# Kernel optimization log

Measured on AMD Instinct MI355X. Metric: run time of the kernel, lower is better.

The kernel has to match this reference:

```python
import jax, jax.numpy as jnp
import numpy as np

B_, C_, H_, W_ = 16, 128, 64, 64
D_MODEL = C_ // 4          # 32
D_STATE = 16
D_CONV = 4
EXPAND = 2
D_INNER = EXPAND * D_MODEL # 64
DT_RANK = (D_MODEL + 15) // 16  # 2
EPS = 1e-5


def setup_inputs() -> dict:
    key = jax.random.key(0)
    ks = jax.random.split(key, 8)
    def n(k, shape, scale=0.02):
        return jax.random.normal(k, shape, dtype=jnp.float32) * scale
    A = jnp.broadcast_to(jnp.arange(1, D_STATE + 1, dtype=jnp.float32), (D_INNER, D_STATE))
    return {
        "input":     jax.random.normal(ks[0], (B_, C_, H_, W_), dtype=jnp.float32),
        "ln_g":      jnp.ones((C_,), jnp.float32),
        "ln_b":      jnp.zeros((C_,), jnp.float32),
        "in_proj_w": n(ks[1], (2 * D_INNER, D_MODEL)),
        "conv_w":    n(ks[2], (D_INNER, D_CONV), 0.1),
        "conv_b":    jnp.zeros((D_INNER,), jnp.float32),
        "x_proj_w":  n(ks[3], (DT_RANK + 2 * D_STATE, D_INNER)),
        "dt_proj_w": n(ks[4], (D_INNER, DT_RANK), 0.5),
        "dt_proj_b": jnp.full((D_INNER,), -4.6, jnp.float32),  # softplus^-1(~0.01)
        "A_log":     jnp.log(A),
        "D":         jnp.ones((D_INNER,), jnp.float32),
        "out_proj_w": n(ks[5], (D_MODEL, D_INNER)),
    }


def _mamba(x, in_proj_w, conv_w, conv_b, x_proj_w, dt_proj_w, dt_proj_b, A_log, D, out_proj_w):
    # x: (G, L, d_model); G = 4 chunks * batch, shared weights -> one big batched call
    G, L, _ = x.shape
    xz = jnp.einsum('gld,ed->gle', x, in_proj_w)          # (G, L, 2*d_inner)
    xi, z = jnp.split(xz, 2, axis=-1)
    # causal depthwise conv1d along L
    xc = jax.lax.conv_general_dilated(
        xi.transpose(0, 2, 1),                            # (G, d_inner, L)
        conv_w[:, None, :],                               # (d_inner, 1, k)
        window_strides=(1,), padding=[(D_CONV - 1, 0)],
        feature_group_count=D_INNER)
    u = jax.nn.silu(xc.transpose(0, 2, 1) + conv_b)       # (G, L, d_inner)
    x_dbl = jnp.einsum('gld,ed->gle', u, x_proj_w)        # (G, L, dt_rank + 2*d_state)
    dt, Bm, Cm = jnp.split(x_dbl, [DT_RANK, DT_RANK + D_STATE], axis=-1)
    delta = jax.nn.softplus(jnp.einsum('glr,dr->gld', dt, dt_proj_w) + dt_proj_b)
    A = -jnp.exp(A_log)                                   # (d_inner, d_state)

    def step(h, inputs):
        d_t, u_t, B_t, C_t = inputs                       # (G,d) (G,d) (G,n) (G,n)
        dA = jnp.exp(d_t[..., None] * A)                  # (G, d, n)
        h = h * dA + (d_t * u_t)[..., None] * B_t[:, None, :]
        y = jnp.einsum('gdn,gn->gd', h, C_t)
        return h, y

    h0 = jnp.zeros((G, D_INNER, D_STATE), x.dtype)
    xs = (delta.transpose(1, 0, 2), u.transpose(1, 0, 2),
          Bm.transpose(1, 0, 2), Cm.transpose(1, 0, 2))
    _, ys = jax.lax.scan(step, h0, xs)                    # ys: (L, G, d_inner)
    y = ys.transpose(1, 0, 2) + u * D
    y = y * jax.nn.silu(z)
    return jnp.einsum('gld,ed->gle', y, out_proj_w)       # (G, L, d_model)


def reference(input, ln_g, ln_b, in_proj_w, conv_w, conv_b, x_proj_w,
              dt_proj_w, dt_proj_b, A_log, D, out_proj_w):
    B, C, H, W = input.shape
    L = H * W
    xf = input.reshape(B, C, L).transpose(0, 2, 1)        # (B, L, C)
    mu = xf.mean(-1, keepdims=True)
    var = ((xf - mu) ** 2).mean(-1, keepdims=True)
    xn = (xf - mu) / jnp.sqrt(var + EPS) * ln_g + ln_b
    # chunk channels into 4 groups (torch.chunk dim=2) and batch them for one mamba call
    chunks = xn.reshape(B, L, 4, C // 4).transpose(2, 0, 1, 3).reshape(4 * B, L, C // 4)
    y = chunks + _mamba(chunks, in_proj_w, conv_w, conv_b, x_proj_w,
                        dt_proj_w, dt_proj_b, A_log, D, out_proj_w)
    out = y.reshape(4, B, L, C // 4).transpose(1, 2, 0, 3).reshape(B, L, C)
    return out.transpose(0, 2, 1).reshape(B, C, H, W)
```

## Files before the change

kernel.cpp:

```cpp
#include <hip/hip_runtime.h>
#include <hip/hip_bf16.h>
#include <hip/hip_fp16.h>
#include <math.h>

typedef __hip_bfloat16 bf;
typedef float f2 __attribute__((ext_vector_type(2)));
typedef _Float16 hf2 __attribute__((ext_vector_type(2)));

#define BB   16
#define CC   128
#define LL   4096
#define DM   32
#define DI   64
#define DSN  16
#define GG   64
#define NC   128
#define CL   32
#define TLV  61
#define NT   68
#define XS   133
#define YS   35
#define XROW 20

__device__ __forceinline__ float bf2f(bf x) { return __bfloat162float(x); }
__device__ __forceinline__ bf f2bf(float x) { return __float2bfloat16(x); }
__device__ __forceinline__ float blo(unsigned v) { return __uint_as_float(v << 16); }
__device__ __forceinline__ float bhi(unsigned v) { return __uint_as_float(v & 0xffff0000u); }
__device__ __forceinline__ float us2f(unsigned short v) { return __uint_as_float((unsigned)v << 16); }
__device__ __forceinline__ unsigned pack2(float a, float b) {
  bf ba = f2bf(a), bb = f2bf(b);
  unsigned short ua = *(unsigned short*)&ba, ub = *(unsigned short*)&bb;
  return (unsigned)ua | ((unsigned)ub << 16);
}
__device__ __forceinline__ unsigned pack2h(float a, float b) {
  _Float16 ha = (_Float16)a, hb = (_Float16)b;
  unsigned short ua = *(unsigned short*)&ha, ub = *(unsigned short*)&hb;
  return (unsigned)ua | ((unsigned)ub << 16);
}
__device__ __forceinline__ hf2 u2h2(unsigned v) {
  union { unsigned u; hf2 h; } c; c.u = v; return c.h;
}

#if __has_builtin(__builtin_amdgcn_exp2f)
#define EXP2F(x) __builtin_amdgcn_exp2f(x)
#else
#define EXP2F(x) exp2f(x)
#endif

#if __has_builtin(__builtin_amdgcn_fdot2)
#define FDOT2(a, b, c) __builtin_amdgcn_fdot2((a), (b), (c), false)
#else
#define FDOT2(a, b, c) ((c) + (float)(a).x * (float)(b).x + (float)(a).y * (float)(b).y)
#endif

__device__ __forceinline__ float sigmoidf_(float x) { return 1.0f / (1.0f + __expf(-x)); }
__device__ __forceinline__ float softplus_fast(float x) {
  float t = EXP2F(-fabsf(x) * 1.44269504088896f);
  return fmaxf(x, 0.0f) + 0.69314718056f * __log2f(1.0f + t);
}

__global__ __launch_bounds__(256, 4) void k1_ln_conv(
    const float* __restrict__ input, const float* __restrict__ ln_g, const float* __restrict__ ln_b,
    const float* __restrict__ in_proj_w, const float* __restrict__ conv_w, const float* __restrict__ conv_b,
    bf* __restrict__ u_ws, bf* __restrict__ xn_ws) {
  __shared__ unsigned ldsbuf[8960];
  __shared__ float mu_s[64], rs_s[64];
  float* xnT = (float*)ldsbuf;
  unsigned short* xiS = (unsigned short*)ldsbuf;
  int b = blockIdx.x / NT;
  int tile = blockIdx.x - b * NT;
  int l0 = tile * TLV;
  int tid = threadIdx.x;
  const float* inb = input + (size_t)b * CC * LL;
#pragma unroll
  for (int k = 0; k < 32; k++) {
    int i = tid + k * 256;
    int j = i & 63, c = i >> 6;
    int l = l0 - 3 + j;
    xnT[j * XS + c] = (l >= 0 && l < LL) ? inb[c * LL + l] : 0.0f;
  }
  __syncthreads();
  if (tid < 64) {
    float s = 0.f, s2 = 0.f;
    for (int c = 0; c < CC; c++) { float v = xnT[tid * XS + c]; s += v; s2 = fmaf(v, v, s2); }
    float mu = s * (1.0f / CC);
    float var = s2 * (1.0f / CC) - mu * mu;
    mu_s[tid] = mu;
    rs_s[tid] = rsqrtf(var + 1e-5f);
  }
  __syncthreads();
#pragma unroll
  for (int k = 0; k < 32; k++) {
    int i = tid + k * 256;
    int j = i & 63, c = i >> 6;
    xnT[j * XS + c] = (xnT[j * XS + c] - mu_s[j]) * rs_s[j] * ln_g[c] + ln_b[c];
  }
  __syncthreads();
  for (int i = tid; i < CC * TLV; i += 256) {
    int c = i / TLV, j2 = i - c * TLV;
    int l = l0 + j2;
    if (l < LL) xn_ws[((size_t)(b * CC + c)) * LL + l] = f2bf(xnT[(j2 + 3) * XS + c]);
  }
  int g = tid >> 6, j = tid & 63;
  float xr[32];
#pragma unroll
  for (int r = 0; r < 32; r++) xr[r] = xnT[j * XS + g * DM + r];
  bool zero_col = (l0 - 3 + j < 0);
  __syncthreads();
#pragma unroll
  for (int c2 = 0; c2 < 4; c2++) {
    float acc[16];
#pragma unroll
    for (int dd = 0; dd < 16; dd++) {
      const float* w = in_proj_w + (c2 * 16 + dd) * DM;
      float a = 0.f;
#pragma unroll
      for (int r = 0; r < 32; r++) a = fmaf(xr[r], w[r], a);
      acc[dd] = zero_col ? 0.f : a;
    }
    unsigned* xo = (unsigned*)&ldsbuf[(g * 64 + j) * YS + c2 * 8];
#pragma unroll
    for (int k = 0; k < 8; k++)
      xo[k] = pack2(acc[2 * k], acc[2 * k + 1]);
  }
  __syncthreads();
  int d = j;
  float cw0 = conv_w[d * 4 + 0], cw1 = conv_w[d * 4 + 1];
  float cw2 = conv_w[d * 4 + 2], cw3 = conv_w[d * 4 + 3];
  float cb = conv_b[d];
  bf* uo = u_ws + (size_t)(g * BB + b) * LL * DI + d;
  float x3 = 0.f, x2 = 0.f, x1 = 0.f, x0 = 0.f;
  for (int jj = 0; jj < 64; jj++) {
    float xi = us2f(xiS[(g * 64 + jj) * (2 * YS) + d]);
    x3 = x2; x2 = x1; x1 = x0; x0 = xi;
    int l = l0 + jj - 3;
    if (jj >= 3 && l < LL) {
      float pre = x3 * cw0 + x2 * cw1 + x1 * cw2 + x0 * cw3 + cb;
      float uu = pre * sigmoidf_(pre);
      uo[(size_t)l * DI] = f2bf(uu);
    }
  }
}

__global__ __launch_bounds__(256) void k2_xproj(
    const bf* __restrict__ u_ws, const float* __restrict__ x_proj_w,
    unsigned* __restrict__ xdbl) {
  __shared__ unsigned uS[256 * 33];
  int tid = threadIdx.x;
  size_t pos0 = (size_t)blockIdx.x * 256;
  const unsigned* src = (const unsigned*)u_ws + pos0 * 32;
#pragma unroll
  for (int k = 0; k < 32; k++) {
    int idx = tid + k * 256;
    uS[(idx >> 5) * 33 + (idx & 31)] = src[idx];
  }
  __syncthreads();
  float xdb[34];
#pragma unroll
  for (int e = 0; e < 34; e++) xdb[e] = 0.f;
#pragma unroll
  for (int c2 = 0; c2 < 4; c2++) {
    float f[16];
#pragma unroll
    for (int k = 0; k < 8; k++) {
      unsigned v = uS[tid * 33 + c2 * 8 + k];
      f[2 * k] = blo(v); f[2 * k + 1] = bhi(v);
    }
#pragma unroll
    for (int e = 0; e < 34; e++) {
      const float* w = x_proj_w + e * DI + c2 * 16;
      float a = xdb[e];
#pragma unroll
      for (int i = 0; i < 16; i++) a = fmaf(f[i], w[i], a);
      xdb[e] = a;
    }
  }
  unsigned* row = &uS[tid * 33];
  row[0] = pack2(xdb[0], xdb[1]);
#pragma unroll
  for (int n = 0; n < 8; n++) row[4 + n]  = pack2h(xdb[2 + 2 * n], xdb[3 + 2 * n]);
#pragma unroll
  for (int n = 0; n < 8; n++) row[12 + n] = pack2h(xdb[18 + 2 * n], xdb[19 + 2 * n]);
  __syncthreads();
  unsigned* dst = xdbl + pos0 * XROW;
#pragma unroll
  for (int k = 0; k < XROW; k++) {
    int idx = tid + k * 256;
    int r = idx / XROW, c = idx - r * XROW;
    dst[idx] = uS[r * 33 + c];
  }
}

__device__ __forceinline__ bool ladder_check(const float* A_log, int d, float a0) {
  bool ok = true;
#pragma unroll
  for (int n = 1; n < DSN; n++) {
    float an = -__expf(A_log[d * DSN + n]) * 1.44269504088896f;
    ok = ok && (fabsf(an / a0 - (float)(n + 1)) < 1e-3f);
  }
  return ok;
}

__global__ __launch_bounds__(256, 8) void k3_scanA(
    const unsigned* __restrict__ xdbl, const bf* __restrict__ u_ws,
    const float* __restrict__ A_log, const float* __restrict__ dt_proj_w,
    const float* __restrict__ dt_proj_b,
    __half* __restrict__ hloc, __half* __restrict__ ssum_ws) {
  __shared__ __align__(16) unsigned bS3[4 * 256];
  __shared__ unsigned dtS3[4 * 32];
  int tid = threadIdx.x;
  int wv = __builtin_amdgcn_readfirstlane(tid >> 6);
  int wid = __builtin_amdgcn_readfirstlane(blockIdx.x * 4 + wv);
  int s = wid >> 7, chunk = wid & (NC - 1);
  int d = tid & 63;
  float a0 = -__expf(A_log[d * DSN]) * 1.44269504088896f;
  bool ok = ladder_check(A_log, d, a0);
  float w0 = dt_proj_w[2 * d], w1 = dt_proj_w[2 * d + 1], bd = dt_proj_b[d];
  hf2 h2[8];
#pragma unroll
  for (int p2 = 0; p2 < 8; p2++) h2[p2] = u2h2(0u);
  float ss = 0.f;
  size_t base = (size_t)s * LL + (size_t)chunk * CL;
  const unsigned short* up = (const unsigned short*)u_ws + base * DI + d;
  const unsigned* xrow = xdbl + base * XROW;
  int wb = wv * 256, wd3 = wv * 32;
#pragma unroll
  for (int k = 0; k < 4; k++) {
    int jj2 = k * 64 + d;
    bS3[wb + jj2] = xrow[(jj2 >> 3) * XROW + 4 + (jj2 & 7)];
  }
  if (d < 32) dtS3[wd3 + d] = xrow[d * XROW];
  if (ok) {
    for (int t = 0; t < CL; t++) {
      unsigned dtp = dtS3[wd3 + t];
      uint4 bA = *(const uint4*)&bS3[wb + t * 8];
      uint4 bB = *(const uint4*)&bS3[wb + t * 8 + 4];
      float x = fmaf(bhi(dtp), w1, fmaf(blo(dtp), w0, bd));
      float delta = softplus_fast(x);
      float uu = us2f(up[(size_t)t * DI]);
      float du = delta * uu;
      ss += delta;
      float E = EXP2F(delta * a0);
      float E2 = E * E;
      hf2 e2; e2.x = (_Float16)E; e2.y = (_Float16)E2;
      hf2 E22; E22.x = (_Float16)E2; E22.y = (_Float16)E2;
      _Float16 duh = (_Float16)du;
      hf2 du2; du2.x = duh; du2.y = duh;
      unsigned bw[8] = {bA.x, bA.y, bA.z, bA.w, bB.x, bB.y, bB.z, bB.w};
#pragma unroll
      for (int p2 = 0; p2 < 8; p2++) {
        hf2 Bp = u2h2(bw[p2]);
        h2[p2] = h2[p2] * e2 + Bp * du2;
        e2 = e2 * E22;
      }
    }
  } else {
    f2 A2p[8];
#pragma unroll
    for (int p2 = 0; p2 < 8; p2++) {
      A2p[p2].x = -__expf(A_log[d * DSN + 2 * p2]) * 1.44269504088896f;
      A2p[p2].y = -__expf(A_log[d * DSN + 2 * p2 + 1]) * 1.44269504088896f;
    }
    for (int t = 0; t < CL; t++) {
      unsigned dtp = dtS3[wd3 + t];
      uint4 bA = *(const uint4*)&bS3[wb + t * 8];
      uint4 bB = *(const uint4*)&bS3[wb + t * 8 + 4];
      float x = fmaf(bhi(dtp), w1, fmaf(blo(dtp), w0, bd));
      float delta = softplus_fast(x);
      float uu = us2f(up[(size_t)t * DI]);
      float du = delta * uu;
      ss += delta;
      _Float16 duh = (_Float16)du;
      hf2 du2; du2.x = duh; du2.y = duh;
      unsigned bw[8] = {bA.x, bA.y, bA.z, bA.w, bB.x, bB.y, bB.z, bB.w};
#pragma unroll
      for (int p2 = 0; p2 < 8; p2++) {
        hf2 ee; ee.x = (_Float16)EXP2F(delta * A2p[p2].x); ee.y = (_Float16)EXP2F(delta * A2p[p2].y);
        hf2 Bp = u2h2(bw[p2]);
        h2[p2] = h2[p2] * ee + Bp * du2;
      }
    }
  }
  size_t ob = (size_t)wid * (DSN * DI) + d;
  unsigned short* hl = (unsigned short*)hloc;
#pragma unroll
  for (int n = 0; n < DSN; n++) {
    _Float16 v = (n & 1) ? h2[n >> 1].y : h2[n >> 1].x;
    hl[ob + n * DI] = *(unsigned short*)&v;
  }
  ssum_ws[wid * DI + d] = __float2half(ss);
}

__global__ __launch_bounds__(256) void k4_combine(
    const __half* __restrict__ ssum_ws, const float* __restrict__ A_log, __half* hloc_hin) {
  int s = blockIdx.x >> 2;
  int q = blockIdx.x & 3;
  int tid = threadIdx.x;
  int n = q * 4 + (tid >> 6);
  int d = tid & 63;
  float A2 = -__expf(A_log[d * DSN + n]) * 1.44269504088896f;
  float h = 0.f;
  const __half* sp = ssum_ws + (size_t)s * NC * DI + d;
  __half* hp = hloc_hin + (size_t)s * NC * (DSN * DI) + n * DI + d;
  float hl[4], ssv[4], hln[4], ssn[4];
#pragma unroll
  for (int j = 0; j < 4; j++) {
    hln[j] = __half2float(hp[(size_t)j * (DSN * DI)]);
    ssn[j] = __half2float(sp[j * DI]);
  }
  for (int kb = 0; kb < NC / 4; kb++) {
#pragma unroll
    for (int j = 0; j < 4; j++) { hl[j] = hln[j]; ssv[j] = ssn[j]; }
    if (kb + 1 < NC / 4) {
#pragma unroll
      for (int j = 0; j < 4; j++) {
        int k = (kb + 1) * 4 + j;
        hln[j] = __half2float(hp[(size_t)k * (DSN * DI)]);
        ssn[j] = __half2float(sp[k * DI]);
      }
    }
#pragma unroll
    for (int j = 0; j < 4; j++) {
      int k = kb * 4 + j;
      float ap = EXP2F(A2 * ssv[j]);
      hp[(size_t)k * (DSN * DI)] = __float2half(h);
      h = fmaf(h, ap, hl[j]);
    }
  }
}

__global__ __launch_bounds__(512, 4) void k56_scan_final(
    const unsigned* __restrict__ xdbl, const bf* __restrict__ u_ws,
    const float* __restrict__ A_log, const float* __restrict__ dt_proj_w,
    const float* __restrict__ dt_proj_b, const float* __restrict__ Dw,
    const __half* __restrict__ hin, const bf* __restrict__ xn_ws,
    const float* __restrict__ in_proj_w, const float* __restrict__ out_proj_w,
    float* __restrict__ out) {
  __shared__ unsigned y2S[4 * 64 * 33];
  __shared__ __align__(16) unsigned bcS[8 * 512];
  __shared__ unsigned dtS[8 * 32];
  int b = blockIdx.x >> 6;
  int cpair = blockIdx.x & 63;
  int l0b = cpair * 64;
  int tid = threadIdx.x;
  int w = __builtin_amdgcn_readfirstlane(tid >> 6);
  int g = w >> 1, half = w & 1;
  int d = tid & 63;
  int chunk = cpair * 2 + half;
  int s_u = __builtin_amdgcn_readfirstlane(g * BB + b);
  float a0 = -__expf(A_log[d * DSN]) * 1.44269504088896f;
  bool ok = ladder_check(A_log, d, a0);
  float w0 = dt_proj_w[2 * d], w1 = dt_proj_w[2 * d + 1], bd = dt_proj_b[d];
  float Dd = Dw[d];
  size_t hb = (size_t)(s_u * NC + chunk) * (DSN * DI) + d;
  const unsigned short* hinus = (const unsigned short*)hin;
  hf2 h2[8];
#pragma unroll
  for (int p2 = 0; p2 < 8; p2++) {
    unsigned lo = hinus[hb + (size_t)(2 * p2) * DI];
    unsigned hi = hinus[hb + (size_t)(2 * p2 + 1) * DI];
    h2[p2] = u2h2(lo | (hi << 16));
  }
  size_t base = (size_t)s_u * LL + (size_t)chunk * CL;
  const unsigned short* up = (const unsigned short*)u_ws + base * DI + d;
  const unsigned* xrow = xdbl + base * XROW;
  int wbc = w * 512, wdt = w * 32;
#pragma unroll
  for (int k = 0; k < 8; k++) {
    int jj2 = k * 64 + d;
    bcS[wbc + jj2] = xrow[(jj2 >> 4) * XROW + 4 + (jj2 & 15)];
  }
  if (d < 32) dtS[wdt + d] = xrow[d * XROW];
  unsigned short* yout = (unsigned short*)y2S + g * 4224 + (half * CL) * 66 + d;
  if (ok) {
    for (int t = 0; t < CL; t++) {
      unsigned dtp = dtS[wdt + t];
      uint4 bA = *(const uint4*)&bcS[wbc + t * 16];
      uint4 bB = *(const uint4*)&bcS[wbc + t * 16 + 4];
      uint4 cA = *(const uint4*)&bcS[wbc + t * 16 + 8];
      uint4 cB = *(const uint4*)&bcS[wbc + t * 16 + 12];
      float x = fmaf(bhi(dtp), w1, fmaf(blo(dtp), w0, bd));
      float delta = softplus_fast(x);
      float uu = us2f(up[(size_t)t * DI]);
      float du = delta * uu;
      float E = EXP2F(delta * a0);
      float E2 = E * E;
      hf2 e2; e2.x = (_Float16)E; e2.y = (_Float16)E2;
      hf2 E22; E22.x = (_Float16)E2; E22.y = (_Float16)E2;
      _Float16 duh = (_Float16)du;
      hf2 du2; du2.x = duh; du2.y = duh;
      float yacc = 0.f;
      unsigned bw[8] = {bA.x, bA.y, bA.z, bA.w, bB.x, bB.y, bB.z, bB.w};
      unsigned cw[8] = {cA.x, cA.y, cA.z, cA.w, cB.x, cB.y, cB.z, cB.w};
#pragma unroll
      for (int p2 = 0; p2 < 8; p2++) {
        hf2 Bp = u2h2(bw[p2]);
        hf2 Cp = u2h2(cw[p2]);
        h2[p2] = h2[p2] * e2 + Bp * du2;
        yacc = FDOT2(h2[p2], Cp, yacc);
        e2 = e2 * E22;
      }
      bf rv = f2bf(yacc + uu * Dd);
      yout[t * 66] = *(unsigned short*)&rv;
    }
  } else {
    f2 A2p[8];
#pragma unroll
    for (int p2 = 0; p2 < 8; p2++) {
      A2p[p2].x = -__expf(A_log[d * DSN + 2 * p2]) * 1.44269504088896f;
      A2p[p2].y = -__expf(A_log[d * DSN + 2 * p2 + 1]) * 1.44269504088896f;
    }
    for (int t = 0; t < CL; t++) {
      unsigned dtp = dtS[wdt + t];
      uint4 bA = *(const uint4*)&bcS[wbc + t * 16];
      uint4 bB = *(const uint4*)&bcS[wbc + t * 16 + 4];
      uint4 cA = *(const uint4*)&bcS[wbc + t * 16 + 8];
      uint4 cB = *(const uint4*)&bcS[wbc + t * 16 + 12];
      float x = fmaf(bhi(dtp), w1, fmaf(blo(dtp), w0, bd));
      float delta = softplus_fast(x);
      float uu = us2f(up[(size_t)t * DI]);
      float du = delta * uu;
      _Float16 duh = (_Float16)du;
      hf2 du2; du2.x = duh; du2.y = duh;
      float yacc = 0.f;
      unsigned bw[8] = {bA.x, bA.y, bA.z, bA.w, bB.x, bB.y, bB.z, bB.w};
      unsigned cw[8] = {cA.x, cA.y, cA.z, cA.w, cB.x, cB.y, cB.z, cB.w};
#pragma unroll
      for (int p2 = 0; p2 < 8; p2++) {
        hf2 ee; ee.x = (_Float16)EXP2F(delta * A2p[p2].x); ee.y = (_Float16)EXP2F(delta * A2p[p2].y);
        hf2 Bp = u2h2(bw[p2]);
        hf2 Cp = u2h2(cw[p2]);
        h2[p2] = h2[p2] * ee + Bp * du2;
        yacc = FDOT2(h2[p2], Cp, yacc);
      }
      bf rv = f2bf(yacc + uu * Dd);
      yout[t * 66] = *(unsigned short*)&rv;
    }
  }
  __syncthreads();
  int p = half;
  int j = d;
  const unsigned short* xnp = (const unsigned short*)xn_ws
                            + ((size_t)(b * CC + g * DM)) * LL + l0b + j;
  float acc[32];
#pragma unroll
  for (int dd = 0; dd < 32; dd++) acc[dd] = 0.f;
#pragma unroll
  for (int c4 = 0; c4 < 4; c4++) {
    float xc[8];
#pragma unroll
    for (int r8 = 0; r8 < 8; r8++)
      xc[r8] = us2f(xnp[(size_t)(c4 * 8 + r8) * LL]);
#pragma unroll
    for (int dd = 0; dd < 32; dd++) {
      const float* wz = in_proj_w + (DI + p * 32 + dd) * DM + c4 * 8;
      float a = acc[dd];
#pragma unroll
      for (int r8 = 0; r8 < 8; r8++) a = fmaf(xc[r8], wz[r8], a);
      acc[dd] = a;
    }
  }
  const unsigned* yrow = y2S + g * 2112 + j * 33;
#pragma unroll
  for (int kk = 0; kk < 16; kk++) {
    unsigned v = yrow[p * 16 + kk];
    float z0 = acc[2 * kk], z1 = acc[2 * kk + 1];
    acc[2 * kk]     = blo(v) * (z0 * sigmoidf_(z0));
    acc[2 * kk + 1] = bhi(v) * (z1 * sigmoidf_(z1));
  }
  __syncthreads();
  float* prow = (float*)y2S + g * 2112 + j * 33;
  int jjb = (1 - p) * 16;
#pragma unroll
  for (int jj = 0; jj < 16; jj++) {
    const float* wo = out_proj_w + (jjb + jj) * DI + p * 32;
    float a = 0.f;
#pragma unroll
    for (int dd = 0; dd < 32; dd++) a = fmaf(acc[dd], wo[dd], a);
    prow[jjb + jj] = a;
  }
  __syncthreads();
  int jf = p * 16;
  float* ob = out + ((size_t)(b * CC + g * DM)) * LL + l0b + j;
#pragma unroll
  for (int jj = 0; jj < 16; jj++) {
    const float* wo = out_proj_w + (jf + jj) * DI + p * 32;
    float a = us2f(xnp[(size_t)(jf + jj) * LL]) + prow[jf + jj];
#pragma unroll
    for (int dd = 0; dd < 32; dd++) a = fmaf(acc[dd], wo[dd], a);
    ob[(size_t)(jf + jj) * LL] = a;
  }
}

extern "C" void kernel_launch(void* const* d_in, const int* in_sizes, int n_in,
                              void* d_out, int out_size, void* d_ws, size_t ws_size,
                              hipStream_t stream) {
  const float* input     = (const float*)d_in[0];
  const float* ln_g      = (const float*)d_in[1];
  const float* ln_b      = (const float*)d_in[2];
  const float* in_proj_w = (const float*)d_in[3];
  const float* conv_w    = (const float*)d_in[4];
  const float* conv_b    = (const float*)d_in[5];
  const float* x_proj_w  = (const float*)d_in[6];
  const float* dt_proj_w = (const float*)d_in[7];
  const float* dt_proj_b = (const float*)d_in[8];
  const float* A_log     = (const float*)d_in[9];
  const float* Dw        = (const float*)d_in[10];
  const float* out_proj_w= (const float*)d_in[11];
  float* out = (float*)d_out;

  char* ws = (char*)d_ws;
  bf*       u_ws  = (bf*)(ws);
  unsigned* xdbl  = (unsigned*)(ws + 33554432);
  bf*       xn_ws = (bf*)(ws + 54525952);
  __half*   hloc  = (__half*)(ws + 71303168);
  __half*   ssum  = (__half*)(ws + 88080384);
  (void)in_sizes; (void)n_in; (void)out_size; (void)ws_size;

  hipLaunchKernelGGL(k1_ln_conv, dim3(BB * NT), dim3(256), 0, stream,
                     input, ln_g, ln_b, in_proj_w, conv_w, conv_b, u_ws, xn_ws);
  hipLaunchKernelGGL(k2_xproj, dim3(1024), dim3(256), 0, stream,
                     u_ws, x_proj_w, xdbl);
  hipLaunchKernelGGL(k3_scanA, dim3(GG * NC / 4), dim3(256), 0, stream,
                     xdbl, u_ws, A_log, dt_proj_w, dt_proj_b, hloc, ssum);
  hipLaunchKernelGGL(k4_combine, dim3(GG * 4), dim3(256), 0, stream,
                     ssum, A_log, hloc);
  hipLaunchKernelGGL(k56_scan_final, dim3(BB * NC / 2), dim3(512), 0, stream,
                     xdbl, u_ws, A_log, dt_proj_w, dt_proj_b, Dw, hloc, xn_ws,
                     in_proj_w, out_proj_w, out);
}
```

Measured before the change: 364.1 us.

## Fuse chunk-local scan into x_proj kernel reading B/dt from shared memory

Merges the chunk-local state scan (old k3) into the x_proj kernel. Each 256-position block now scans its own 8 chunks of 32 steps straight from the packed x_dbl rows already in shared memory, with each wave handling two chunks. This removes one kernel launch and the global re-read of x_dbl for the scan. In exchange the scan runs with less parallelism per block (two sequential chunks per wave instead of one) and strided, likely bank-conflicted LDS reads (row stride 33).

```diff
diff --git a/kernel.cpp b/kernel.cpp
--- a/kernel.cpp
+++ b/kernel.cpp
@@ -59,6 +59,16 @@
   return fmaxf(x, 0.0f) + 0.69314718056f * __log2f(1.0f + t);
 }
 
+__device__ __forceinline__ bool ladder_check(const float* A_log, int d, float a0) {
+  bool ok = true;
+#pragma unroll
+  for (int n = 1; n < DSN; n++) {
+    float an = -__expf(A_log[d * DSN + n]) * 1.44269504088896f;
+    ok = ok && (fabsf(an / a0 - (float)(n + 1)) < 1e-3f);
+  }
+  return ok;
+}
+
 __global__ __launch_bounds__(256, 4) void k1_ln_conv(
     const float* __restrict__ input, const float* __restrict__ ln_g, const float* __restrict__ ln_b,
     const float* __restrict__ in_proj_w, const float* __restrict__ conv_w, const float* __restrict__ conv_b,
@@ -144,7 +154,9 @@
 
 __global__ __launch_bounds__(256) void k2_xproj(
     const bf* __restrict__ u_ws, const float* __restrict__ x_proj_w,
-    unsigned* __restrict__ xdbl) {
+    const float* __restrict__ A_log, const float* __restrict__ dt_proj_w,
+    const float* __restrict__ dt_proj_b,
+    unsigned* __restrict__ xdbl, __half* __restrict__ hloc, __half* __restrict__ ssum_ws) {
   __shared__ unsigned uS[256 * 33];
   int tid = threadIdx.x;
   size_t pos0 = (size_t)blockIdx.x * 256;
@@ -189,106 +201,78 @@
     int r = idx / XROW, c = idx - r * XROW;
     dst[idx] = uS[r * 33 + c];
   }
-}
-
-__device__ __forceinline__ bool ladder_check(const float* A_log, int d, float a0) {
-  bool ok = true;
-#pragma unroll
-  for (int n = 1; n < DSN; n++) {
-    float an = -__expf(A_log[d * DSN + n]) * 1.44269504088896f;
-    ok = ok && (fabsf(an / a0 - (float)(n + 1)) < 1e-3f);
-  }
-  return ok;
-}
-
-__global__ __launch_bounds__(256, 8) void k3_scanA(
-    const unsigned* __restrict__ xdbl, const bf* __restrict__ u_ws,
-    const float* __restrict__ A_log, const float* __restrict__ dt_proj_w,
-    const float* __restrict__ dt_proj_b,
-    __half* __restrict__ hloc, __half* __restrict__ ssum_ws) {
-  __shared__ __align__(16) unsigned bS3[4 * 256];
-  __shared__ unsigned dtS3[4 * 32];
-  int tid = threadIdx.x;
-  int wv = __builtin_amdgcn_readfirstlane(tid >> 6);
-  int wid = __builtin_amdgcn_readfirstlane(blockIdx.x * 4 + wv);
-  int s = wid >> 7, chunk = wid & (NC - 1);
-  int d = tid & 63;
+  int wv = tid >> 6, d = tid & 63;
+  int s = (int)(pos0 >> 12);
+  int ch0 = (int)((pos0 & (LL - 1)) >> 5);
   float a0 = -__expf(A_log[d * DSN]) * 1.44269504088896f;
   bool ok = ladder_check(A_log, d, a0);
   float w0 = dt_proj_w[2 * d], w1 = dt_proj_w[2 * d + 1], bd = dt_proj_b[d];
-  hf2 h2[8];
-#pragma unroll
-  for (int p2 = 0; p2 < 8; p2++) h2[p2] = u2h2(0u);
-  float ss = 0.f;
-  size_t base = (size_t)s * LL + (size_t)chunk * CL;
-  const unsigned short* up = (const unsigned short*)u_ws + base * DI + d;
-  const unsigned* xrow = xdbl + base * XROW;
-  int wb = wv * 256, wd3 = wv * 32;
-#pragma unroll
-  for (int k = 0; k < 4; k++) {
-    int jj2 = k * 64 + d;
-    bS3[wb + jj2] = xrow[(jj2 >> 3) * XROW + 4 + (jj2 & 7)];
-  }
-  if (d < 32) dtS3[wd3 + d] = xrow[d * XROW];
-  if (ok) {
-    for (int t = 0; t < CL; t++) {
-      unsigned dtp = dtS3[wd3 + t];
-      uint4 bA = *(const uint4*)&bS3[wb + t * 8];
-      uint4 bB = *(const uint4*)&bS3[wb + t * 8 + 4];
-      float x = fmaf(bhi(dtp), w1, fmaf(blo(dtp), w0, bd));
-      float delta = softplus_fast(x);
-      float uu = us2f(up[(size_t)t * DI]);
-      float du = delta * uu;
-      ss += delta;
-      float E = EXP2F(delta * a0);
-      float E2 = E * E;
-      hf2 e2; e2.x = (_Float16)E; e2.y = (_Float16)E2;
-      hf2 E22; E22.x = (_Float16)E2; E22.y = (_Float16)E2;
-      _Float16 duh = (_Float16)du;
-      hf2 du2; du2.x = duh; du2.y = duh;
-      unsigned bw[8] = {bA.x, bA.y, bA.z, bA.w, bB.x, bB.y, bB.z, bB.w};
+  unsigned short* hl = (unsigned short*)hloc;
+  for (int cc = 0; cc < 2; cc++) {
+    int lch = wv * 2 + cc;
+    int wid = s * NC + ch0 + lch;
+    hf2 h2[8];
+#pragma unroll
+    for (int p2 = 0; p2 < 8; p2++) h2[p2] = u2h2(0u);
+    float ss = 0.f;
+    const unsigned short* up = (const unsigned short*)u_ws
+                             + (pos0 + (size_t)lch * CL) * DI + d;
+    const unsigned* rowb = &uS[lch * CL * 33];
+    if (ok) {
+      for (int t = 0; t < CL; t++) {
+        const unsigned* r = rowb + t * 33;
+        unsigned dtp = r[0];
+        float x = fmaf(bhi(dtp), w1, fmaf(blo(dtp), w0, bd));
+        float delta = softplus_fast(x);
+        float uu = us2f(up[(size_t)t * DI]);
+        float du = delta * uu;
+        ss += delta;
+        float E = EXP2F(delta * a0);
+        float E2 = E * E;
+        hf2 e2; e2.x = (_Float16)E; e2.y = (_Float16)E2;
+        hf2 E22; E22.x = (_Float16)E2; E22.y = (_Float16)E2;
+        _Float16 duh = (_Float16)du;
+        hf2 du2; du2.x = duh; du2.y = duh;
+#pragma unroll
+        for (int p2 = 0; p2 < 8; p2++) {
+          hf2 Bp = u2h2(r[4 + p2]);
+          h2[p2] = h2[p2] * e2 + Bp * du2;
+          e2 = e2 * E22;
+        }
+      }
+    } else {
+      f2 A2p[8];
 #pragma unroll
       for (int p2 = 0; p2 < 8; p2++) {
-        hf2 Bp = u2h2(bw[p2]);
-        h2[p2] = h2[p2] * e2 + Bp * du2;
-        e2 = e2 * E22;
+        A2p[p2].x = -__expf(A_log[d * DSN + 2 * p2]) * 1.44269504088896f;
+        A2p[p2].y = -__expf(A_log[d * DSN + 2 * p2 + 1]) * 1.44269504088896f;
       }
-    }
-  } else {
-    f2 A2p[8];
-#pragma unroll
-    for (int p2 = 0; p2 < 8; p2++) {
-      A2p[p2].x = -__expf(A_log[d * DSN + 2 * p2]) * 1.44269504088896f;
-      A2p[p2].y = -__expf(A_log[d * DSN + 2 * p2 + 1]) * 1.44269504088896f;
-    }
-    for (int t = 0; t < CL; t++) {
-      unsigned dtp = dtS3[wd3 + t];
-      uint4 bA = *(const uint4*)&bS3[wb + t * 8];
-      uint4 bB = *(const uint4*)&bS3[wb + t * 8 + 4];
-      float x = fmaf(bhi(dtp), w1, fmaf(blo(dtp), w0, bd));
-      float delta = softplus_fast(x);
-      float uu = us2f(up[(size_t)t * DI]);
-      float du = delta * uu;
-      ss += delta;
-      _Float16 duh = (_Float16)du;
-      hf2 du2; du2.x = duh; du2.y = duh;
-      unsigned bw[8] = {bA.x, bA.y, bA.z, bA.w, bB.x, bB.y, bB.z, bB.w};
-#pragma unroll
-      for (int p2 = 0; p2 < 8; p2++) {
-        hf2 ee; ee.x = (_Float16)EXP2F(delta * A2p[p2].x); ee.y = (_Float16)EXP2F(delta * A2p[p2].y);
-        hf2 Bp = u2h2(bw[p2]);
-        h2[p2] = h2[p2] * ee + Bp * du2;
+      for (int t = 0; t < CL; t++) {
+        const unsigned* r = rowb + t * 33;
+        unsigned dtp = r[0];
+        float x = fmaf(bhi(dtp), w1, fmaf(blo(dtp), w0, bd));
+        float delta = softplus_fast(x);
+        float uu = us2f(up[(size_t)t * DI]);
+        float du = delta * uu;
+        ss += delta;
+        _Float16 duh = (_Float16)du;
+        hf2 du2; du2.x = duh; du2.y = duh;
+#pragma unroll
+        for (int p2 = 0; p2 < 8; p2++) {
+          hf2 ee; ee.x = (_Float16)EXP2F(delta * A2p[p2].x); ee.y = (_Float16)EXP2F(delta * A2p[p2].y);
+          hf2 Bp = u2h2(r[4 + p2]);
+          h2[p2] = h2[p2] * ee + Bp * du2;
+        }
       }
     }
-  }
-  size_t ob = (size_t)wid * (DSN * DI) + d;
-  unsigned short* hl = (unsigned short*)hloc;
-#pragma unroll
-  for (int n = 0; n < DSN; n++) {
-    _Float16 v = (n & 1) ? h2[n >> 1].y : h2[n >> 1].x;
-    hl[ob + n * DI] = *(unsigned short*)&v;
-  }
-  ssum_ws[wid * DI + d] = __float2half(ss);
+    size_t ob = (size_t)wid * (DSN * DI) + d;
+#pragma unroll
+    for (int n = 0; n < DSN; n++) {
+      _Float16 v = (n & 1) ? h2[n >> 1].y : h2[n >> 1].x;
+      hl[ob + n * DI] = *(unsigned short*)&v;
+    }
+    ssum_ws[wid * DI + d] = __float2half(ss);
+  }
 }
 
 __global__ __launch_bounds__(256) void k4_combine(
@@ -520,9 +504,7 @@
   hipLaunchKernelGGL(k1_ln_conv, dim3(BB * NT), dim3(256), 0, stream,
                      input, ln_g, ln_b, in_proj_w, conv_w, conv_b, u_ws, xn_ws);
   hipLaunchKernelGGL(k2_xproj, dim3(1024), dim3(256), 0, stream,
-                     u_ws, x_proj_w, xdbl);
-  hipLaunchKernelGGL(k3_scanA, dim3(GG * NC / 4), dim3(256), 0, stream,
-                     xdbl, u_ws, A_log, dt_proj_w, dt_proj_b, hloc, ssum);
+                     u_ws, x_proj_w, A_log, dt_proj_w, dt_proj_b, xdbl, hloc, ssum);
   hipLaunchKernelGGL(k4_combine, dim3(GG * 4), dim3(256), 0, stream,
                      ssum, A_log, hloc);
   hipLaunchKernelGGL(k56_scan_final, dim3(BB * NC / 2), dim3(512), 0, stream,
```

Measured after the change: 350.4 us, median of 2. -3.8%, faster.
